# Kernel optimization log

Measured on AMD Instinct MI355X. Metric: run time of the kernel, lower is better.

The kernel has to match this reference:

```python
import jax, jax.numpy as jnp
import numpy as np

# ---- static module config (matches torch defaults) ----
N_LEVELS = 16
MIN_RES = 16
MAX_RES = 512
N_ENC = 2 ** 14
D = 3          # n_input_dims
E = 2          # n_embed_dims
B = 1 << 20    # number of query points

# per-level resolutions, computed in float32 to mirror torch's float32 log/exp
_gf = np.exp((np.log(np.float32(MAX_RES)) - np.log(np.float32(MIN_RES))) / np.float32(N_LEVELS - 1)).astype(np.float32)
RES = [int(np.floor(np.float32(MIN_RES) * _gf ** np.float32(l))) for l in range(N_LEVELS)]
DIRECT = [r ** D < N_ENC for r in RES]                  # small grids use direct ravel indexing
NLE = [min(r ** D, N_ENC) for r in RES]                  # encodings per level (sentinel row at index NLE[l])

# 2^D corner offsets, shape (8, 3)
OFFS = np.stack(np.meshgrid(*([np.arange(2)] * D), indexing='ij'), axis=-1).reshape(-1, D).astype(np.int32)
# instant-ngp spatial hashing primes
PRIMES = (1, 2654435761, 805459861)


def setup_inputs() -> dict:
    key = jax.random.key(0)
    k1, k2 = jax.random.split(key)
    x = jax.random.uniform(k1, (B, D), dtype=jnp.float32, minval=-1.0, maxval=1.0)
    # stacked per-level tables, padded to (N_ENC+1, E); rows >= NLE[l] zeroed
    emb = jax.random.uniform(k2, (N_LEVELS, N_ENC + 1, E), dtype=jnp.float32, minval=-1e-4, maxval=1e-4)
    row = np.arange(N_ENC + 1)
    valid = (row[None, :] < np.asarray(NLE)[:, None])    # (L, N_ENC+1); also zeroes the sentinel row
    emb = emb * jnp.asarray(valid[..., None], dtype=jnp.float32)
    return {"x": x, "emb": emb}


def _level_features(x, emb_l, R, n_encs, direct):
    offs = jnp.asarray(OFFS)                             # (8, 3)
    xs = (x + 1.0) * (R * 0.5) - 0.5                     # grid coords
    xl = jnp.floor(xs)
    frac = xs - xl                                       # (B, 3)
    xi = xl.astype(jnp.int32)
    c = xi[:, None, :] + offs[None, :, :]                # (B, 8, 3) corner indices
    # bilinear/trilinear weights: prod over dims of frac (offset=1) or 1-frac (offset=0)
    w = jnp.prod(jnp.where(offs[None].astype(bool), frac[:, None, :], 1.0 - frac[:, None, :]), axis=-1)  # (B, 8)
    w = jax.lax.stop_gradient(w)                         # torch computes weights under no_grad
    m = jnp.all((c >= 0) & (c < R), axis=-1)             # (B, 8) corner validity
    if direct:
        ids = (c[..., 0] * R + c[..., 1]) * R + c[..., 2]
    else:
        cu = c.astype(jnp.uint32)
        h = (cu[..., 0] * jnp.uint32(PRIMES[0])
             ^ cu[..., 1] * jnp.uint32(PRIMES[1])
             ^ cu[..., 2] * jnp.uint32(PRIMES[2]))
        ids = (h % jnp.uint32(n_encs)).astype(jnp.int32)
    ids = jnp.where(m, ids, n_encs)                      # invalid corners -> zero sentinel row
    return jnp.sum(emb_l[ids] * w[..., None], axis=1)    # (B, E)


def reference(x, emb):
    feats = [
        _level_features(x, emb[l], RES[l], NLE[l], DIRECT[l])
        for l in range(N_LEVELS)
    ]
    return jnp.stack(feats, axis=1)                      # (B, L, E)
```

## Files before the change

### kernel.cpp

```cpp
#include <hip/hip_runtime.h>
#include <hip/hip_fp16.h>


typedef __attribute__((ext_vector_type(2))) float f32x2;

#define B_POINTS (1 << 20)
#define N_LEVELS 16
#define TAB_F2   16385
#define WG       1024
#define NWG      256
#define NPAIR    8
#define NCHUNK   (NWG / NPAIR)
#define CHUNK    (B_POINTS / NCHUNK)
#define PPT      (CHUNK / WG)
#define GRP      4
#define NGRP     (PPT / GRP)

__constant__ int   cRES[N_LEVELS]  = {16, 20, 25, 32, 40, 50, 64, 80,
                                      101, 128, 161, 203, 256, 322, 406, 512};
__constant__ float cHALF[N_LEVELS] = {8.f, 10.f, 12.5f, 16.f, 20.f, 25.f, 32.f, 40.f,
                                      50.5f, 64.f, 80.5f, 101.5f, 128.f, 161.f, 203.f, 256.f};
__constant__ int   cROWS[N_LEVELS] = {4096, 8000, 15625, 16384, 16384, 16384, 16384, 16384,
                                      16384, 16384, 16384, 16384, 16384, 16384, 16384, 16384};
__constant__ int   cBASE[N_LEVELS] = {0, 4096, 16384, 0, 0, 16384, 0, 16384,
                                      0, 16384, 0, 16384, 0, 16384, 0, 16384};

__device__ __forceinline__ void level_feat(const char* __restrict__ tb,
                                           float cx, float cy, float cz,
                                           int R, int Rm1, float half, float hb,
                                           bool direct, unsigned base4,
                                           float& acc0, float& acc1)
{
    const float xs0 = fmaf(cx, half, hb);
    const float xs1 = fmaf(cy, half, hb);
    const float xs2 = fmaf(cz, half, hb);
    const float fl0 = floorf(xs0), fl1 = floorf(xs1), fl2 = floorf(xs2);
    const float f0 = xs0 - fl0, f1 = xs1 - fl1, f2 = xs2 - fl2;
    const float g0 = 1.0f - f0, g1 = 1.0f - f1, g2 = 1.0f - f2;
    const int i0 = (int)fl0, i1 = (int)fl1, i2 = (int)fl2;

    const float wx0 = (i0 >= 0)  ? g0 : 0.0f;
    const float wx1 = (i0 < Rm1) ? f0 : 0.0f;
    const float wy0 = (i1 >= 0)  ? g1 : 0.0f;
    const float wy1 = (i1 < Rm1) ? f1 : 0.0f;
    const float wz0 = (i2 >= 0)  ? g2 : 0.0f;
    const float wz1 = (i2 < Rm1) ? f2 : 0.0f;

    const float pxy00 = wx0 * wy0, pxy01 = wx0 * wy1;
    const float pxy10 = wx1 * wy0, pxy11 = wx1 * wy1;
    const float w0 = pxy00 * wz0, w1 = pxy00 * wz1;
    const float w2 = pxy01 * wz0, w3 = pxy01 * wz1;
    const float w4 = pxy10 * wz0, w5 = pxy10 * wz1;
    const float w6 = pxy11 * wz0, w7 = pxy11 * wz1;

    unsigned d0, d1, d2, d3, d4, d5, d6, d7;
    if (direct) {
        const int R4  = R * 4;
        const int RR4 = R * R * 4;
        const int u0l = max(i0, 0), u0h = min(i0 + 1, Rm1);
        const int u1l = max(i1, 0), u1h = min(i1 + 1, Rm1);
        const int u2l = max(i2, 0), u2h = min(i2 + 1, Rm1);
        const int a0  = u0l * RR4 + (int)base4, a1 = u0h * RR4 + (int)base4;
        const int b00 = a0 + u1l * R4, b01 = a0 + u1h * R4;
        const int b10 = a1 + u1l * R4, b11 = a1 + u1h * R4;
        const int zl  = u2l * 4,       zh  = u2h * 4;
        d0 = b00 + zl; d1 = b00 + zh; d2 = b01 + zl; d3 = b01 + zh;
        d4 = b10 + zl; d5 = b10 + zh; d6 = b11 + zl; d7 = b11 + zh;
    } else {
        const unsigned MB  = 16383u << 2;
        const unsigned hx0 = (unsigned)i0 << 2,                 hx1 = hx0 + 4u;
        const unsigned hy0 = (unsigned)i1 * (2654435761u * 4u), hy1 = hy0 + (2654435761u * 4u);
        const unsigned hzf = (unsigned)i2 * (805459861u * 4u);
        const unsigned hz0 = (hzf & MB) | base4;
        const unsigned hz1 = ((hzf + (805459861u * 4u)) & MB) | base4;
        const unsigned t00 = (hx0 ^ hy0) & MB, t01 = (hx0 ^ hy1) & MB;
        const unsigned t10 = (hx1 ^ hy0) & MB, t11 = (hx1 ^ hy1) & MB;
        d0 = t00 ^ hz0; d1 = t00 ^ hz1; d2 = t01 ^ hz0; d3 = t01 ^ hz1;
        d4 = t10 ^ hz0; d5 = t10 ^ hz1; d6 = t11 ^ hz0; d7 = t11 ^ hz1;
    }

    const __half2 e0 = *(const __half2*)(tb + d0);
    const __half2 e1 = *(const __half2*)(tb + d1);
    const __half2 e2 = *(const __half2*)(tb + d2);
    const __half2 e3 = *(const __half2*)(tb + d3);
    const __half2 e4 = *(const __half2*)(tb + d4);
    const __half2 e5 = *(const __half2*)(tb + d5);
    const __half2 e6 = *(const __half2*)(tb + d6);
    const __half2 e7 = *(const __half2*)(tb + d7);
    acc0 = 0.0f; acc1 = 0.0f;
    acc0 = fmaf(__low2float(e0),  w0, acc0); acc1 = fmaf(__high2float(e0), w0, acc1);
    acc0 = fmaf(__low2float(e1),  w1, acc0); acc1 = fmaf(__high2float(e1), w1, acc1);
    acc0 = fmaf(__low2float(e2),  w2, acc0); acc1 = fmaf(__high2float(e2), w2, acc1);
    acc0 = fmaf(__low2float(e3),  w3, acc0); acc1 = fmaf(__high2float(e3), w3, acc1);
    acc0 = fmaf(__low2float(e4),  w4, acc0); acc1 = fmaf(__high2float(e4), w4, acc1);
    acc0 = fmaf(__low2float(e5),  w5, acc0); acc1 = fmaf(__high2float(e5), w5, acc1);
    acc0 = fmaf(__low2float(e6),  w6, acc0); acc1 = fmaf(__high2float(e6), w6, acc1);
    acc0 = fmaf(__low2float(e7),  w7, acc0); acc1 = fmaf(__high2float(e7), w7, acc1);
}

__device__ __forceinline__ void stage_level(__half2* __restrict__ tab,
                                            const f32x2* __restrict__ src,
                                            int rows, int obase, int t)
{
    for (int r0 = 0; r0 < rows; r0 += 4 * WG) {
        f32x2 v[4];
#pragma unroll
        for (int u = 0; u < 4; ++u) {
            const int r = r0 + u * WG + t;
            if (r < rows) v[u] = src[r];
        }
#pragma unroll
        for (int u = 0; u < 4; ++u) {
            const int r = r0 + u * WG + t;
            if (r < rows) {
                __half2 h;
                h.x = __float2half_rn(v[u].x);
                h.y = __float2half_rn(v[u].y);
                tab[obase + r] = h;
            }
        }
    }
}

__global__ __launch_bounds__(WG, 4)
void hashenc_pair(const float* __restrict__ x,
                  const float* __restrict__ emb,
                  float* __restrict__ out)
{
    __shared__ __half2 tab[32768];

    const int bid = blockIdx.x;
    const int xcd = bid & 7;
    const int s   = bid >> 3;
    const int m   = s & 7;
    const int c   = ((s >> 3) << 3) | xcd;

    const int lA = 2 * m, lB = 2 * m + 1;
    const int   RA = cRES[lA],  RB = cRES[lB];
    const int   RmA = RA - 1,   RmB = RB - 1;
    const float hA = cHALF[lA], hB = cHALF[lB];
    const float bA = hA - 0.5f, bB = hB - 0.5f;
    const bool  dA = (lA < 3),  dB = (lB < 3);
    const unsigned baseA = (unsigned)cBASE[lA] * 4u;
    const unsigned baseB = (unsigned)cBASE[lB] * 4u;

    const int t    = threadIdx.x;
    const int base = c * CHUNK + t;

    float xa[GRP], xb[GRP], xcv[GRP];
#pragma unroll
    for (int j = 0; j < GRP; ++j) {
        const float3 v = ((const float3*)x)[base + j * WG];
        xa[j] = v.x; xb[j] = v.y; xcv[j] = v.z;
    }

    stage_level(tab, (const f32x2*)emb + (size_t)lA * TAB_F2, cROWS[lA], cBASE[lA], t);
    stage_level(tab, (const f32x2*)emb + (size_t)lB * TAB_F2, cROWS[lB], cBASE[lB], t);
    __syncthreads();

    const char* tb = (const char*)tab;

    for (int kg = 0; kg < NGRP; ++kg) {
        float ca[GRP], cb[GRP], cc[GRP];
#pragma unroll
        for (int j = 0; j < GRP; ++j) { ca[j] = xa[j]; cb[j] = xb[j]; cc[j] = xcv[j]; }

        if (kg + 1 < NGRP) {
#pragma unroll
            for (int j = 0; j < GRP; ++j) {
                const float3 v = ((const float3*)x)[base + (kg + 1) * (GRP * WG) + j * WG];
                xa[j] = v.x; xb[j] = v.y; xcv[j] = v.z;
            }
        }

#pragma unroll
        for (int j = 0; j < GRP; ++j) {
            const int p = base + kg * (GRP * WG) + j * WG;

            float a0, a1, b0, b1;
            level_feat(tb, ca[j], cb[j], cc[j], RA, RmA, hA, bA, dA, baseA, a0, a1);
            level_feat(tb, ca[j], cb[j], cc[j], RB, RmB, hB, bB, dB, baseB, b0, b1);

            ((float4*)out)[(size_t)p * NPAIR + m] = make_float4(a0, a1, b0, b1);
        }
    }
}

extern "C" void kernel_launch(void* const* d_in, const int* in_sizes, int n_in,
                              void* d_out, int out_size, void* d_ws, size_t ws_size,
                              hipStream_t stream) {
    const float* x   = (const float*)d_in[0];
    const float* emb = (const float*)d_in[1];
    float* out = (float*)d_out;

    hashenc_pair<<<NWG, WG, 0, stream>>>(x, emb, out);
}
```

Before: 203.1 us.

## Split encoding into per-level kernel with fp16 workspace plus transpose kernel

Each block now handles a single level, so it stages a 64KB LDS table instead of the 128KB needed for two levels, which allows two 1024-thread blocks per CU. Results go to a level-major fp16 workspace, and a second kernel transposes them through LDS into the interleaved fp32 output. The goal is better latency hiding for the random LDS gathers. In exchange it adds about 128MB of extra workspace traffic, reads x twice as often, and rounds outputs to fp16. The old fused kernel is kept as a fallback when no workspace is supplied.

```diff
diff --git a/kernel.cpp b/kernel.cpp
--- a/kernel.cpp
+++ b/kernel.cpp
@@ -8,13 +8,17 @@
 #define N_LEVELS 16
 #define TAB_F2   16385
 #define WG       1024
-#define NWG      256
-#define NPAIR    8
-#define NCHUNK   (NWG / NPAIR)
+
+#define NWG      512
+#define NCHUNK   (NWG / N_LEVELS)
 #define CHUNK    (B_POINTS / NCHUNK)
 #define PPT      (CHUNK / WG)
 #define GRP      4
 #define NGRP     (PPT / GRP)
+
+#define T_WG     256
+#define T_TILE   256
+#define T_NWG    (B_POINTS / T_TILE)
 
 __constant__ int   cRES[N_LEVELS]  = {16, 20, 25, 32, 40, 50, 64, 80,
                                       101, 128, 161, 203, 256, 322, 406, 512};
@@ -25,6 +29,166 @@
 __constant__ int   cBASE[N_LEVELS] = {0, 4096, 16384, 0, 0, 16384, 0, 16384,
                                       0, 16384, 0, 16384, 0, 16384, 0, 16384};
 
+__global__ __launch_bounds__(WG, 8)
+void hashenc_lvl(const float* __restrict__ x,
+                 const float* __restrict__ emb,
+                 __half2* __restrict__ ws)
+{
+    __shared__ __half2 tab[16384];
+
+    const int bid = blockIdx.x;
+    const int xcd = bid & 7;
+    const int s   = bid >> 3;
+    const int l   = s & 15;
+    const int c   = ((s >> 4) << 3) | xcd;
+
+    const int   R      = cRES[l];
+    const int   Rm1    = R - 1;
+    const float half   = cHALF[l];
+    const float hb     = half - 0.5f;
+    const bool  direct = (l < 3);
+    const int   R4     = R * 4;
+    const int   RR4    = R * R * 4;
+
+    const f32x2* __restrict__ gtab = (const f32x2*)emb + (size_t)l * TAB_F2;
+    const int t    = threadIdx.x;
+    const int base = c * CHUNK + t;
+
+    float xa[GRP], xb[GRP], xcv[GRP];
+#pragma unroll
+    for (int j = 0; j < GRP; ++j) {
+        const float3 v = ((const float3*)x)[base + j * WG];
+        xa[j] = v.x; xb[j] = v.y; xcv[j] = v.z;
+    }
+
+#pragma unroll
+    for (int j = 0; j < 16; ++j) {
+        const f32x2 v = gtab[j * WG + t];
+        __half2 h;
+        h.x = __float2half_rn(v.x);
+        h.y = __float2half_rn(v.y);
+        tab[j * WG + t] = h;
+    }
+    __syncthreads();
+
+    const char* tb = (const char*)tab;
+    __half2* __restrict__ wsl = ws + (size_t)l * B_POINTS;
+
+    for (int kg = 0; kg < NGRP; ++kg) {
+        float ca[GRP], cb[GRP], cc[GRP];
+#pragma unroll
+        for (int j = 0; j < GRP; ++j) { ca[j] = xa[j]; cb[j] = xb[j]; cc[j] = xcv[j]; }
+
+        if (kg + 1 < NGRP) {
+#pragma unroll
+            for (int j = 0; j < GRP; ++j) {
+                const float3 v = ((const float3*)x)[base + (kg + 1) * (GRP * WG) + j * WG];
+                xa[j] = v.x; xb[j] = v.y; xcv[j] = v.z;
+            }
+        }
+
+#pragma unroll
+        for (int j = 0; j < GRP; ++j) {
+            const int p = base + kg * (GRP * WG) + j * WG;
+
+            const float xs0 = fmaf(ca[j], half, hb);
+            const float xs1 = fmaf(cb[j], half, hb);
+            const float xs2 = fmaf(cc[j], half, hb);
+            const float fl0 = floorf(xs0), fl1 = floorf(xs1), fl2 = floorf(xs2);
+            const float f0 = xs0 - fl0, f1 = xs1 - fl1, f2 = xs2 - fl2;
+            const float g0 = 1.0f - f0, g1 = 1.0f - f1, g2 = 1.0f - f2;
+            const int i0 = (int)fl0, i1 = (int)fl1, i2 = (int)fl2;
+
+            const float wx0 = (i0 >= 0)  ? g0 : 0.0f;
+            const float wx1 = (i0 < Rm1) ? f0 : 0.0f;
+            const float wy0 = (i1 >= 0)  ? g1 : 0.0f;
+            const float wy1 = (i1 < Rm1) ? f1 : 0.0f;
+            const float wz0 = (i2 >= 0)  ? g2 : 0.0f;
+            const float wz1 = (i2 < Rm1) ? f2 : 0.0f;
+
+            const float pxy00 = wx0 * wy0, pxy01 = wx0 * wy1;
+            const float pxy10 = wx1 * wy0, pxy11 = wx1 * wy1;
+            const float w0 = pxy00 * wz0, w1 = pxy00 * wz1;
+            const float w2 = pxy01 * wz0, w3 = pxy01 * wz1;
+            const float w4 = pxy10 * wz0, w5 = pxy10 * wz1;
+            const float w6 = pxy11 * wz0, w7 = pxy11 * wz1;
+
+            unsigned d0, d1, d2, d3, d4, d5, d6, d7;
+            if (direct) {
+                const int u0l = max(i0, 0), u0h = min(i0 + 1, Rm1);
+                const int u1l = max(i1, 0), u1h = min(i1 + 1, Rm1);
+                const int u2l = max(i2, 0), u2h = min(i2 + 1, Rm1);
+                const int a0  = u0l * RR4,     a1  = u0h * RR4;
+                const int b00 = a0 + u1l * R4, b01 = a0 + u1h * R4;
+                const int b10 = a1 + u1l * R4, b11 = a1 + u1h * R4;
+                const int zl  = u2l * 4,       zh  = u2h * 4;
+                d0 = b00 + zl; d1 = b00 + zh; d2 = b01 + zl; d3 = b01 + zh;
+                d4 = b10 + zl; d5 = b10 + zh; d6 = b11 + zl; d7 = b11 + zh;
+            } else {
+                const unsigned MB  = 16383u << 2;
+                const unsigned hx0 = (unsigned)i0 << 2,                 hx1 = hx0 + 4u;
+                const unsigned hy0 = (unsigned)i1 * (2654435761u * 4u), hy1 = hy0 + (2654435761u * 4u);
+                const unsigned hzf = (unsigned)i2 * (805459861u * 4u);
+                const unsigned hz0 = hzf & MB, hz1 = (hzf + (805459861u * 4u)) & MB;
+                const unsigned t00 = (hx0 ^ hy0) & MB, t01 = (hx0 ^ hy1) & MB;
+                const unsigned t10 = (hx1 ^ hy0) & MB, t11 = (hx1 ^ hy1) & MB;
+                d0 = t00 ^ hz0; d1 = t00 ^ hz1; d2 = t01 ^ hz0; d3 = t01 ^ hz1;
+                d4 = t10 ^ hz0; d5 = t10 ^ hz1; d6 = t11 ^ hz0; d7 = t11 ^ hz1;
+            }
+
+            float acc0 = 0.0f, acc1 = 0.0f;
+            const __half2 e0 = *(const __half2*)(tb + d0);
+            const __half2 e1 = *(const __half2*)(tb + d1);
+            const __half2 e2 = *(const __half2*)(tb + d2);
+            const __half2 e3 = *(const __half2*)(tb + d3);
+            const __half2 e4 = *(const __half2*)(tb + d4);
+            const __half2 e5 = *(const __half2*)(tb + d5);
+            const __half2 e6 = *(const __half2*)(tb + d6);
+            const __half2 e7 = *(const __half2*)(tb + d7);
+            acc0 = fmaf(__low2float(e0),  w0, acc0); acc1 = fmaf(__high2float(e0), w0, acc1);
+            acc0 = fmaf(__low2float(e1),  w1, acc0); acc1 = fmaf(__high2float(e1), w1, acc1);
+            acc0 = fmaf(__low2float(e2),  w2, acc0); acc1 = fmaf(__high2float(e2), w2, acc1);
+            acc0 = fmaf(__low2float(e3),  w3, acc0); acc1 = fmaf(__high2float(e3), w3, acc1);
+            acc0 = fmaf(__low2float(e4),  w4, acc0); acc1 = fmaf(__high2float(e4), w4, acc1);
+            acc0 = fmaf(__low2float(e5),  w5, acc0); acc1 = fmaf(__high2float(e5), w5, acc1);
+            acc0 = fmaf(__low2float(e6),  w6, acc0); acc1 = fmaf(__high2float(e6), w6, acc1);
+            acc0 = fmaf(__low2float(e7),  w7, acc0); acc1 = fmaf(__high2float(e7), w7, acc1);
+
+            wsl[p] = __floats2half2_rn(acc0, acc1);
+        }
+    }
+}
+
+__global__ __launch_bounds__(T_WG)
+void out_transpose(const __half2* __restrict__ ws, float4* __restrict__ out4)
+{
+    __shared__ unsigned lds[T_TILE * 17];
+    const int p0 = blockIdx.x * T_TILE;
+    const int t  = threadIdx.x;
+
+#pragma unroll
+    for (int j = 0; j < (T_TILE * N_LEVELS / 2) / T_WG; ++j) {
+        const int u   = j * T_WG + t;
+        const int l   = u >> 7;
+        const int pl2 = u & 127;
+        const uint2 w2 = ((const uint2*)(ws + (size_t)l * B_POINTS + p0))[pl2];
+        lds[(2 * pl2)     * 17 + l] = w2.x;
+        lds[(2 * pl2 + 1) * 17 + l] = w2.y;
+    }
+    __syncthreads();
+
+#pragma unroll
+    for (int j = 0; j < (T_TILE * 8) / T_WG; ++j) {
+        const int v  = j * T_WG + t;
+        const int pl = v >> 3, lp = v & 7;
+        const __half2 ha = *(const __half2*)&lds[pl * 17 + 2 * lp];
+        const __half2 hb = *(const __half2*)&lds[pl * 17 + 2 * lp + 1];
+        const float2 fa = __half22float2(ha);
+        const float2 fb = __half22float2(hb);
+        out4[(size_t)p0 * 8 + v] = make_float4(fa.x, fa.y, fb.x, fb.y);
+    }
+}
+
 __device__ __forceinline__ void level_feat(const char* __restrict__ tb,
                                            float cx, float cy, float cz,
                                            int R, int Rm1, float half, float hb,
@@ -38,21 +202,18 @@
     const float f0 = xs0 - fl0, f1 = xs1 - fl1, f2 = xs2 - fl2;
     const float g0 = 1.0f - f0, g1 = 1.0f - f1, g2 = 1.0f - f2;
     const int i0 = (int)fl0, i1 = (int)fl1, i2 = (int)fl2;
-
     const float wx0 = (i0 >= 0)  ? g0 : 0.0f;
     const float wx1 = (i0 < Rm1) ? f0 : 0.0f;
     const float wy0 = (i1 >= 0)  ? g1 : 0.0f;
     const float wy1 = (i1 < Rm1) ? f1 : 0.0f;
     const float wz0 = (i2 >= 0)  ? g2 : 0.0f;
     const float wz1 = (i2 < Rm1) ? f2 : 0.0f;
-
     const float pxy00 = wx0 * wy0, pxy01 = wx0 * wy1;
     const float pxy10 = wx1 * wy0, pxy11 = wx1 * wy1;
     const float w0 = pxy00 * wz0, w1 = pxy00 * wz1;
     const float w2 = pxy01 * wz0, w3 = pxy01 * wz1;
     const float w4 = pxy10 * wz0, w5 = pxy10 * wz1;
     const float w6 = pxy11 * wz0, w7 = pxy11 * wz1;
-
     unsigned d0, d1, d2, d3, d4, d5, d6, d7;
     if (direct) {
         const int R4  = R * 4;
@@ -78,7 +239,6 @@
         d0 = t00 ^ hz0; d1 = t00 ^ hz1; d2 = t01 ^ hz0; d3 = t01 ^ hz1;
         d4 = t10 ^ hz0; d5 = t10 ^ hz1; d6 = t11 ^ hz0; d7 = t11 ^ hz1;
     }
-
     const __half2 e0 = *(const __half2*)(tb + d0);
     const __half2 e1 = *(const __half2*)(tb + d1);
     const __half2 e2 = *(const __half2*)(tb + d2);
@@ -128,13 +288,11 @@
                   float* __restrict__ out)
 {
     __shared__ __half2 tab[32768];
-
     const int bid = blockIdx.x;
     const int xcd = bid & 7;
     const int s   = bid >> 3;
     const int m   = s & 7;
     const int c   = ((s >> 3) << 3) | xcd;
-
     const int lA = 2 * m, lB = 2 * m + 1;
     const int   RA = cRES[lA],  RB = cRES[lB];
     const int   RmA = RA - 1,   RmB = RB - 1;
@@ -143,28 +301,22 @@
     const bool  dA = (lA < 3),  dB = (lB < 3);
     const unsigned baseA = (unsigned)cBASE[lA] * 4u;
     const unsigned baseB = (unsigned)cBASE[lB] * 4u;
-
     const int t    = threadIdx.x;
-    const int base = c * CHUNK + t;
-
+    const int base = c * (B_POINTS / 32) + t;
     float xa[GRP], xb[GRP], xcv[GRP];
 #pragma unroll
     for (int j = 0; j < GRP; ++j) {
         const float3 v = ((const float3*)x)[base + j * WG];
         xa[j] = v.x; xb[j] = v.y; xcv[j] = v.z;
     }
-
     stage_level(tab, (const f32x2*)emb + (size_t)lA * TAB_F2, cROWS[lA], cBASE[lA], t);
     stage_level(tab, (const f32x2*)emb + (size_t)lB * TAB_F2, cROWS[lB], cBASE[lB], t);
     __syncthreads();
-
     const char* tb = (const char*)tab;
-
     for (int kg = 0; kg < NGRP; ++kg) {
         float ca[GRP], cb[GRP], cc[GRP];
 #pragma unroll
         for (int j = 0; j < GRP; ++j) { ca[j] = xa[j]; cb[j] = xb[j]; cc[j] = xcv[j]; }
-
         if (kg + 1 < NGRP) {
 #pragma unroll
             for (int j = 0; j < GRP; ++j) {
@@ -172,16 +324,13 @@
                 xa[j] = v.x; xb[j] = v.y; xcv[j] = v.z;
             }
         }
-
 #pragma unroll
         for (int j = 0; j < GRP; ++j) {
             const int p = base + kg * (GRP * WG) + j * WG;
-
             float a0, a1, b0, b1;
             level_feat(tb, ca[j], cb[j], cc[j], RA, RmA, hA, bA, dA, baseA, a0, a1);
             level_feat(tb, ca[j], cb[j], cc[j], RB, RmB, hB, bB, dB, baseB, b0, b1);
-
-            ((float4*)out)[(size_t)p * NPAIR + m] = make_float4(a0, a1, b0, b1);
+            ((float4*)out)[(size_t)p * 8 + m] = make_float4(a0, a1, b0, b1);
         }
     }
 }
@@ -193,5 +342,12 @@
     const float* emb = (const float*)d_in[1];
     float* out = (float*)d_out;
 
-    hashenc_pair<<<NWG, WG, 0, stream>>>(x, emb, out);
-}
+    const size_t ws_need = (size_t)N_LEVELS * B_POINTS * sizeof(__half2);
+    if (d_ws != nullptr && ws_size >= ws_need) {
+        __half2* ws = (__half2*)d_ws;
+        hashenc_lvl<<<NWG, WG, 0, stream>>>(x, emb, ws);
+        out_transpose<<<T_NWG, T_WG, 0, stream>>>(ws, (float4*)out);
+    } else {
+        hashenc_pair<<<256, WG, 0, stream>>>(x, emb, out);
+    }
+}
```

After: 196.5 us. -3.3%, faster.
